# Kernel optimization log

Measured on AMD Instinct MI355X. Metric: run time of the kernel, lower is better.

## Reference

```python
import jax, jax.numpy as jnp
import numpy as np

B, S, D, H = 2, 2048, 1024, 16
HD = D // H

def setup_inputs() -> dict:
    key = jax.random.key(0)
    ks = jax.random.split(key, 9)
    s = 1.0 / np.sqrt(D)
    return {
        "x": jax.random.normal(ks[0], (B, S, D), jnp.float32),
        "Wq": jax.random.uniform(ks[1], (D, D), jnp.float32, -s, s),
        "bq": jax.random.uniform(ks[2], (D,), jnp.float32, -s, s),
        "Wk": jax.random.uniform(ks[3], (D, D), jnp.float32, -s, s),
        "bk": jax.random.uniform(ks[4], (D,), jnp.float32, -s, s),
        "Wv": jax.random.uniform(ks[5], (D, D), jnp.float32, -s, s),
        "bv": jax.random.uniform(ks[6], (D,), jnp.float32, -s, s),
        "Wo": jax.random.uniform(ks[7], (D, D), jnp.float32, -s, s),
        "bo": jax.random.uniform(ks[8], (D,), jnp.float32, -s, s),
    }

def reference(x, Wq, bq, Wk, bk, Wv, bv, Wo, bo):
    b, s, _ = x.shape
    # projections (torch Linear: y = x @ W.T + b; here W stored as [in,out])
    q = x @ Wq + bq
    k = x @ Wk + bk
    v = x @ Wv + bv
    # [b, h, s, hd]
    q = q.reshape(b, s, H, HD).transpose(0, 2, 1, 3)
    k = k.reshape(b, s, H, HD).transpose(0, 2, 1, 3)
    v = v.reshape(b, s, H, HD).transpose(0, 2, 1, 3)
    scores = jnp.einsum("bhqd,bhkd->bhqk", q, k) / jnp.sqrt(jnp.float32(HD))
    weights = jax.nn.softmax(scores, axis=-1)
    attn = jnp.einsum("bhqk,bhkd->bhqd", weights, v)
    attn = attn.transpose(0, 2, 1, 3).reshape(b, s, D)
    return attn @ Wo + bo
```

## Files before the change

kernel.cpp:

```cpp
#include <hip/hip_runtime.h>
#include <hip/hip_bf16.h>
#include <stdint.h>

#define B_  2
#define S_  2048
#define D_  1024
#define H_  16
#define HD_ 64
#define M_  (B_*S_)

typedef __attribute__((ext_vector_type(8)))  short short8;
typedef __attribute__((ext_vector_type(4)))  float f32x4;
typedef __attribute__((ext_vector_type(16))) float f32x16;

__device__ __forceinline__ unsigned short f2bf(float f) {
  union { float f; unsigned int u; } x; x.f = f;
  unsigned int r = (x.u + 0x7FFFu + ((x.u >> 16) & 1u)) >> 16;
  return (unsigned short)r;
}

__device__ __forceinline__ unsigned int pack2(float a, float b) {
  union { float f; unsigned int u; } x, y; x.f = a; y.f = b;
  return __builtin_amdgcn_perm(y.u + 0x8000u, x.u + 0x8000u, 0x07060302u);
}

typedef const __attribute__((address_space(1))) unsigned int* gas1_t;
typedef __attribute__((address_space(3))) unsigned int* las3_t;

__device__ __forceinline__ void gload_lds16(const void* g, void* l) {
  __builtin_amdgcn_global_load_lds((gas1_t)g, (las3_t)l, 16, 0, 0);
}

__global__ void k_cvt_bf16(const float* __restrict__ x, ushort* __restrict__ o, int n4) {
  int i = blockIdx.x * blockDim.x + threadIdx.x;
  int stride = gridDim.x * blockDim.x;
  for (int j = i; j < n4; j += stride) {
    float4 v = ((const float4*)x)[j];
    ushort4 u = make_ushort4(f2bf(v.x), f2bf(v.y), f2bf(v.z), f2bf(v.w));
    ((ushort4*)o)[j] = u;
  }
}

__global__ void k_transpose_w(const float* __restrict__ w0, const float* __restrict__ w1,
                              const float* __restrict__ w2, const float* __restrict__ w3,
                              ushort* __restrict__ o0, ushort* __restrict__ o1,
                              ushort* __restrict__ o2, ushort* __restrict__ o3) {
  const float* w = (blockIdx.z == 0) ? w0 : (blockIdx.z == 1) ? w1 : (blockIdx.z == 2) ? w2 : w3;
  ushort*      o = (blockIdx.z == 0) ? o0 : (blockIdx.z == 1) ? o1 : (blockIdx.z == 2) ? o2 : o3;
  __shared__ float t[32][33];
  int tx = threadIdx.x & 31, ty = threadIdx.x >> 5;
  int kt = blockIdx.y * 32, nt = blockIdx.x * 32;
  #pragma unroll
  for (int i = 0; i < 4; ++i)
    t[ty + 8 * i][tx] = w[(size_t)(kt + ty + 8 * i) * D_ + nt + tx];
  __syncthreads();
  #pragma unroll
  for (int i = 0; i < 4; ++i)
    o[(size_t)(nt + ty + 8 * i) * D_ + kt + tx] = f2bf(t[tx][ty + 8 * i]);
}

__global__ __launch_bounds__(256) void k_gemm_bt(const ushort* __restrict__ A,
                                                 const ushort* __restrict__ Bt,
                                                 const float* __restrict__ b0,
                                                 const float* __restrict__ b1,
                                                 const float* __restrict__ b2,
                                                 void* __restrict__ o0,
                                                 void* __restrict__ o1,
                                                 void* __restrict__ o2, int mode) {
  __shared__ char smem[2][32768];
  const int tid = threadIdx.x;
  const int w = tid >> 6, lane = tid & 63;
  const int g = lane >> 4, c = lane & 15;
  const int m0 = blockIdx.y * 128, n0 = blockIdx.x * 128;
  const int wm = (w >> 1) * 64, wn = (w & 1) * 64;

  f32x4 acc[4][4];
  #pragma unroll
  for (int i = 0; i < 4; ++i)
    #pragma unroll
    for (int j = 0; j < 4; ++j) acc[i][j] = 0.f;

  const char* Abase = (const char*)A + (size_t)m0 * (D_ * 2);
  const char* Bbase = (const char*)Bt + (size_t)n0 * (D_ * 2);

  auto stage = [&](int buf, int kb) {
    char* ls = &smem[buf][0];
    #pragma unroll
    for (int i = 0; i < 4; ++i) {
      int obase = w * 4096 + i * 1024;
      int ot = obase + lane * 16;
      int u = ot ^ (((ot >> 7) & 7) << 4);
      gload_lds16(Abase + (size_t)(u >> 7) * (D_ * 2) + kb * 128 + (u & 127), ls + obase);
    }
    #pragma unroll
    for (int i = 0; i < 4; ++i) {
      int obase = w * 4096 + i * 1024;
      int ot = obase + lane * 16;
      int u = ot ^ (((ot >> 7) & 7) << 4);
      gload_lds16(Bbase + (size_t)(u >> 7) * (D_ * 2) + kb * 128 + (u & 127), ls + 16384 + obase);
    }
  };

  stage(0, 0);
  int cur = 0;
  for (int kb = 0; kb < D_ / 64; ++kb) {
    __syncthreads();
    if (kb < D_ / 64 - 1) stage(cur ^ 1, kb + 1);
    const char* lsA = &smem[cur][0];
    const char* lsB = lsA + 16384;
    short8 a[4][2], b[4][2];
    #pragma unroll
    for (int f = 0; f < 4; ++f) {
      int rowA = wm + f * 16 + c;
      int rowB = wn + f * 16 + c;
      #pragma unroll
      for (int ks = 0; ks < 2; ++ks) {
        int offA = (rowA * 128 + ks * 64 + g * 16) ^ ((rowA & 7) << 4);
        int offB = (rowB * 128 + ks * 64 + g * 16) ^ ((rowB & 7) << 4);
        a[f][ks] = *(const short8*)(lsA + offA);
        b[f][ks] = *(const short8*)(lsB + offB);
      }
    }
    #pragma unroll
    for (int mf = 0; mf < 4; ++mf)
      #pragma unroll
      for (int nf = 0; nf < 4; ++nf) {
        acc[mf][nf] = __builtin_amdgcn_mfma_f32_16x16x32_bf16(a[mf][0], b[nf][0], acc[mf][nf], 0, 0, 0);
        acc[mf][nf] = __builtin_amdgcn_mfma_f32_16x16x32_bf16(a[mf][1], b[nf][1], acc[mf][nf], 0, 0, 0);
      }
    cur ^= 1;
  }

  const int sec = n0 >> 10;
  const float* bb = (mode == 1) ? b0 : (sec == 0) ? b0 : (sec == 1) ? b1 : b2;
  void* outp = (mode == 1) ? o0 : (sec == 0) ? o0 : (sec == 1) ? o1 : o2;
  #pragma unroll
  for (int nf = 0; nf < 4; ++nf) {
    int col = n0 + wn + nf * 16 + c;
    int lc = col & 1023;
    float bvv = bb[lc];
    #pragma unroll
    for (int mf = 0; mf < 4; ++mf) {
      #pragma unroll
      for (int r = 0; r < 4; ++r) {
        int tok = m0 + wm + mf * 16 + 4 * g + r;
        float v = acc[mf][nf][r] + bvv;
        if (mode == 1) {
          ((float*)outp)[(size_t)tok * D_ + col] = v;
        } else {
          if (sec == 0) v *= 0.18033688011112042f;
          int bi = tok >> 11, si = tok & 2047;
          int h = lc >> 6, hd = lc & 63;
          size_t off = (sec == 2)
            ? ((size_t)(bi * H_ + h) * HD_ + hd) * S_ + si
            : ((size_t)(bi * H_ + h) * S_ + si) * HD_ + hd;
          ((ushort*)outp)[off] = f2bf(v);
        }
      }
    }
  }
}

__global__ __launch_bounds__(512, 4) void k_attn(const ushort* __restrict__ Q,
                                                 const ushort* __restrict__ K,
                                                 const ushort* __restrict__ Vt,
                                                 ushort* __restrict__ O) {
  __shared__ __align__(16) char lds[2][2][16384];
  const int tid = threadIdx.x;
  const int w = tid >> 6, lane = tid & 63;
  const int qw = w & 3, g2 = w >> 2;
  const int tl = tid & 255;
  const int ql = lane & 31, hi = lane >> 5;
  const int bid = blockIdx.x;
  const int bh = (bid & 7) * 4 + ((bid >> 3) & 3);
  const int qc = bid >> 5;
  const int q0 = qc * 128 + qw * 32;
  const int kbase = g2 * 1024;
  const ushort* Qb = Q + (size_t)bh * S_ * HD_;
  const char* Kb2 = (const char*)(K + (size_t)bh * S_ * HD_);
  const char* Vb2 = (const char*)(Vt + (size_t)bh * HD_ * S_);

  short8 qf[4];
  #pragma unroll
  for (int t = 0; t < 4; ++t)
    qf[t] = *(const short8*)(Qb + (size_t)(q0 + ql) * HD_ + 16 * t + 8 * hi);

  short8 vones;
  #pragma unroll
  for (int i = 0; i < 8; ++i) vones[i] = (short)0x3F80;

  auto stageKV = [&](int buf, int k0n) {
    char* ls = &lds[buf][g2][0];
    #pragma unroll
    for (int i = 0; i < 2; ++i) {
      int o = tl * 16 + i * 4096;
      int u = o ^ (((o >> 7) & 7) << 4);
      gload_lds16(Kb2 + (size_t)(k0n + (u >> 7)) * 128 + (u & 127), ls + o);
    }
    #pragma unroll
    for (int i = 0; i < 2; ++i) {
      int o = tl * 16 + i * 4096;
      int u = o ^ (((o >> 7) & 7) << 4);
      gload_lds16(Vb2 + (size_t)(u >> 7) * (S_ * 2) + (size_t)k0n * 2 + (u & 127), ls + 8192 + o);
    }
  };

  f32x16 oacc[2], lacc;
  oacc[0] = 0.f; oacc[1] = 0.f; lacc = 0.f;
  float m = -1e30f;

  stageKV(0, kbase);
  int cur = 0;
  for (int kk = 0; kk < 16; ++kk) {
    __syncthreads();
    if (kk < 15) stageKV(cur ^ 1, kbase + (kk + 1) * 64);
    const char* lsK = &lds[cur][g2][0];
    const char* lsV = lsK + 8192;

    f32x16 st[2];
    #pragma unroll
    for (int n = 0; n < 2; ++n) {
      st[n] = 0.f;
      #pragma unroll
      for (int t = 0; t < 4; ++t) {
        int row = 32 * n + ql, col = 32 * t + 16 * hi;
        short8 kf = *(const short8*)(lsK + ((row * 128 + col) ^ ((row & 7) << 4)));
        st[n] = __builtin_amdgcn_mfma_f32_32x32x16_bf16(kf, qf[t], st[n], 0, 0, 0);
      }
    }

    float red[16];
    #pragma unroll
    for (int i = 0; i < 16; ++i) red[i] = fmaxf(st[0][i], st[1][i]);
    #pragma unroll
    for (int s = 8; s >= 1; s >>= 1)
      #pragma unroll
      for (int i = 0; i < s; ++i) red[i] = fmaxf(red[i], red[i + s]);
    float cmax = fmaxf(red[0], __shfl_xor(red[0], 32));

    if (!__all(cmax - m <= 8.0f)) {
      float mnew = fmaxf(m, cmax);
      float sc = exp2f(m - mnew);
      m = mnew;
      #pragma unroll
      for (int i = 0; i < 16; ++i) { oacc[0][i] *= sc; oacc[1][i] *= sc; }
      lacc[0] *= sc;
    }

    short8 pfrag[2][2];
    #pragma unroll
    for (int n = 0; n < 2; ++n) {
      unsigned int pk[4][2];
      #pragma unroll
      for (int b = 0; b < 4; ++b)
        #pragma unroll
        for (int p = 0; p < 2; ++p)
          pk[b][p] = pack2(exp2f(st[n][4 * b + 2 * p] - m), exp2f(st[n][4 * b + 2 * p + 1] - m));
      #pragma unroll
      for (int m2 = 0; m2 < 2; ++m2) {
        union { unsigned int u[4]; short8 v; } fr;
        fr.u[0] = pk[2 * m2][0];     fr.u[1] = pk[2 * m2][1];
        fr.u[2] = pk[2 * m2 + 1][0]; fr.u[3] = pk[2 * m2 + 1][1];
        pfrag[n][m2] = fr.v;
      }
    }

    #pragma unroll
    for (int n = 0; n < 2; ++n)
      #pragma unroll
      for (int m2 = 0; m2 < 2; ++m2)
        lacc = __builtin_amdgcn_mfma_f32_32x32x16_bf16(vones, pfrag[n][m2], lacc, 0, 0, 0);

    #pragma unroll
    for (int dt = 0; dt < 2; ++dt) {
      const int rb = (32 * dt + ql) * 128;
      const int sz = (ql & 7) << 4;
      #pragma unroll
      for (int n = 0; n < 2; ++n)
        #pragma unroll
        for (int m2 = 0; m2 < 2; ++m2) {
          const int cb = 64 * n + 32 * m2 + 8 * hi;
          union { struct { unsigned long long a, b; } q; short8 v; } vf;
          vf.q.a = *(const unsigned long long*)(lsV + ((rb + cb) ^ sz));
          vf.q.b = *(const unsigned long long*)(lsV + ((rb + cb + 16) ^ sz));
          oacc[dt] = __builtin_amdgcn_mfma_f32_32x32x16_bf16(vf.v, pfrag[n][m2], oacc[dt], 0, 0, 0);
        }
    }
    cur ^= 1;
  }

  float l = lacc[0];
  __syncthreads();
  float* fl = (float*)&lds[0][0][0];
  if (g2 == 1) {
    float* ob = fl + (qw * 32 + ql) * 64;
    #pragma unroll
    for (int dt = 0; dt < 2; ++dt)
      #pragma unroll
      for (int rg = 0; rg < 4; ++rg) {
        f32x4 v;
        v[0] = oacc[dt][4 * rg + 0]; v[1] = oacc[dt][4 * rg + 1];
        v[2] = oacc[dt][4 * rg + 2]; v[3] = oacc[dt][4 * rg + 3];
        *(f32x4*)(ob + dt * 32 + rg * 8 + 4 * hi) = v;
      }
    if (hi == 0) {
      fl[8192 + (qw * 32 + ql) * 2 + 0] = m;
      fl[8192 + (qw * 32 + ql) * 2 + 1] = l;
    }
  }
  __syncthreads();
  if (g2 == 0) {
    float mp = fl[8192 + (qw * 32 + ql) * 2 + 0];
    float lp = fl[8192 + (qw * 32 + ql) * 2 + 1];
    float mm = fmaxf(m, mp);
    float a  = exp2f(m - mm), ap = exp2f(mp - mm);
    float invl = 1.f / (l * a + lp * ap);
    const float* ob = fl + (qw * 32 + ql) * 64;
    const int bi = bh >> 4, h = bh & 15;
    const int tok = bi * S_ + q0 + ql;
    #pragma unroll
    for (int dt = 0; dt < 2; ++dt)
      #pragma unroll
      for (int rg = 0; rg < 4; ++rg) {
        f32x4 pv = *(const f32x4*)(ob + dt * 32 + rg * 8 + 4 * hi);
        ushort4 u;
        u.x = f2bf((oacc[dt][4 * rg + 0] * a + pv[0] * ap) * invl);
        u.y = f2bf((oacc[dt][4 * rg + 1] * a + pv[1] * ap) * invl);
        u.z = f2bf((oacc[dt][4 * rg + 2] * a + pv[2] * ap) * invl);
        u.w = f2bf((oacc[dt][4 * rg + 3] * a + pv[3] * ap) * invl);
        *(ushort4*)(O + (size_t)tok * D_ + h * 64 + dt * 32 + rg * 8 + 4 * hi) = u;
      }
  }
}

extern "C" void kernel_launch(void* const* d_in, const int* in_sizes, int n_in,
                              void* d_out, int out_size, void* d_ws, size_t ws_size,
                              hipStream_t stream) {
  const float* x  = (const float*)d_in[0];
  const float* Wq = (const float*)d_in[1];
  const float* bq = (const float*)d_in[2];
  const float* Wk = (const float*)d_in[3];
  const float* bk = (const float*)d_in[4];
  const float* Wv = (const float*)d_in[5];
  const float* bv = (const float*)d_in[6];
  const float* Wo = (const float*)d_in[7];
  const float* bo = (const float*)d_in[8];
  char* ws = (char*)d_ws;
  const size_t MB = 1024 * 1024;
  ushort* Xbf = (ushort*)(ws + 0);
  ushort* Wt3 = (ushort*)(ws + 8 * MB);
  ushort* Wto = (ushort*)(ws + 14 * MB);
  ushort* Qb  = (ushort*)(ws + 16 * MB);
  ushort* Kb  = (ushort*)(ws + 24 * MB);
  ushort* Vtb = (ushort*)(ws + 32 * MB);
  ushort* Att = (ushort*)(ws + 0);

  k_cvt_bf16<<<1024, 256, 0, stream>>>(x, Xbf, M_ * D_ / 4);
  k_transpose_w<<<dim3(32, 32, 4), 256, 0, stream>>>(
      Wq, Wk, Wv, Wo, Wt3, Wt3 + 1024 * 1024, Wt3 + 2048 * 1024, Wto);
  k_gemm_bt<<<dim3(24, 32), 256, 0, stream>>>(Xbf, Wt3, bq, bk, bv, Qb, Kb, Vtb, 0);
  k_attn<<<512, 512, 0, stream>>>(Qb, Kb, Vtb, Att);
  k_gemm_bt<<<dim3(8, 32), 256, 0, stream>>>(Att, Wto, bo, bo, bo, d_out, d_out, d_out, 1);
}
```

Before: 256.9 us.

## Process attention key tile in 32-key halves with a wider LDS swizzle

Splits the per-tile softmax and PV work into two 32-key sub-blocks that each run their own max update, exponentiation and MFMAs, which shortens live ranges and lowers register pressure. Changes the LDS XOR swizzle to mix in higher row bits to cut bank conflicts on K and V reads. Lowers the launch_bounds occupancy hint from 4 to 2, giving the compiler more registers per thread. In exchange, the online rescale check now runs twice per tile, and the lower occupancy can leave less latency hiding.

```diff
diff --git a/kernel.cpp b/kernel.cpp
--- a/kernel.cpp
+++ b/kernel.cpp
@@ -23,6 +23,8 @@
   union { float f; unsigned int u; } x, y; x.f = a; y.f = b;
   return __builtin_amdgcn_perm(y.u + 0x8000u, x.u + 0x8000u, 0x07060302u);
 }
+
+#define SW(row) ((((row) ^ ((row) >> 3)) & 7) << 4)
 
 typedef const __attribute__((address_space(1))) unsigned int* gas1_t;
 typedef __attribute__((address_space(3))) unsigned int* las3_t;
@@ -161,7 +163,7 @@
   }
 }
 
-__global__ __launch_bounds__(512, 4) void k_attn(const ushort* __restrict__ Q,
+__global__ __launch_bounds__(512, 2) void k_attn(const ushort* __restrict__ Q,
                                                  const ushort* __restrict__ K,
                                                  const ushort* __restrict__ Vt,
                                                  ushort* __restrict__ O) {
@@ -194,14 +196,16 @@
     #pragma unroll
     for (int i = 0; i < 2; ++i) {
       int o = tl * 16 + i * 4096;
-      int u = o ^ (((o >> 7) & 7) << 4);
-      gload_lds16(Kb2 + (size_t)(k0n + (u >> 7)) * 128 + (u & 127), ls + o);
+      int row = o >> 7;
+      int u = o ^ SW(row);
+      gload_lds16(Kb2 + (size_t)(k0n + row) * 128 + (u & 127), ls + o);
     }
     #pragma unroll
     for (int i = 0; i < 2; ++i) {
       int o = tl * 16 + i * 4096;
-      int u = o ^ (((o >> 7) & 7) << 4);
-      gload_lds16(Vb2 + (size_t)(u >> 7) * (S_ * 2) + (size_t)k0n * 2 + (u & 127), ls + 8192 + o);
+      int row = o >> 7;
+      int u = o ^ SW(row);
+      gload_lds16(Vb2 + (size_t)row * (S_ * 2) + (size_t)k0n * 2 + (u & 127), ls + 8192 + o);
     }
   };
 
@@ -217,74 +221,63 @@
     const char* lsK = &lds[cur][g2][0];
     const char* lsV = lsK + 8192;
 
-    f32x16 st[2];
     #pragma unroll
     for (int n = 0; n < 2; ++n) {
-      st[n] = 0.f;
+      f32x16 st = 0.f;
       #pragma unroll
       for (int t = 0; t < 4; ++t) {
-        int row = 32 * n + ql, col = 32 * t + 16 * hi;
-        short8 kf = *(const short8*)(lsK + ((row * 128 + col) ^ ((row & 7) << 4)));
-        st[n] = __builtin_amdgcn_mfma_f32_32x32x16_bf16(kf, qf[t], st[n], 0, 0, 0);
-      }
-    }
-
-    float red[16];
-    #pragma unroll
-    for (int i = 0; i < 16; ++i) red[i] = fmaxf(st[0][i], st[1][i]);
-    #pragma unroll
-    for (int s = 8; s >= 1; s >>= 1)
-      #pragma unroll
-      for (int i = 0; i < s; ++i) red[i] = fmaxf(red[i], red[i + s]);
-    float cmax = fmaxf(red[0], __shfl_xor(red[0], 32));
-
-    if (!__all(cmax - m <= 8.0f)) {
-      float mnew = fmaxf(m, cmax);
-      float sc = exp2f(m - mnew);
-      m = mnew;
-      #pragma unroll
-      for (int i = 0; i < 16; ++i) { oacc[0][i] *= sc; oacc[1][i] *= sc; }
-      lacc[0] *= sc;
-    }
-
-    short8 pfrag[2][2];
-    #pragma unroll
-    for (int n = 0; n < 2; ++n) {
-      unsigned int pk[4][2];
-      #pragma unroll
-      for (int b = 0; b < 4; ++b)
+        int row = 32 * n + ql;
+        short8 kf = *(const short8*)(lsK + row * 128 + ((32 * t + 16 * hi) ^ SW(row)));
+        st = __builtin_amdgcn_mfma_f32_32x32x16_bf16(kf, qf[t], st, 0, 0, 0);
+      }
+
+      float red[8];
+      #pragma unroll
+      for (int i = 0; i < 8; ++i) red[i] = fmaxf(st[i], st[i + 8]);
+      #pragma unroll
+      for (int s = 4; s >= 1; s >>= 1)
         #pragma unroll
-        for (int p = 0; p < 2; ++p)
-          pk[b][p] = pack2(exp2f(st[n][4 * b + 2 * p] - m), exp2f(st[n][4 * b + 2 * p + 1] - m));
+        for (int i = 0; i < s; ++i) red[i] = fmaxf(red[i], red[i + s]);
+      float cmax = fmaxf(red[0], __shfl_xor(red[0], 32));
+
+      if (!__all(cmax - m <= 8.0f)) {
+        float mnew = fmaxf(m, cmax);
+        float sc = exp2f(m - mnew);
+        m = mnew;
+        #pragma unroll
+        for (int i = 0; i < 16; ++i) { oacc[0][i] *= sc; oacc[1][i] *= sc; }
+        lacc[0] *= sc;
+      }
+
+      short8 pfrag[2];
       #pragma unroll
       for (int m2 = 0; m2 < 2; ++m2) {
         union { unsigned int u[4]; short8 v; } fr;
-        fr.u[0] = pk[2 * m2][0];     fr.u[1] = pk[2 * m2][1];
-        fr.u[2] = pk[2 * m2 + 1][0]; fr.u[3] = pk[2 * m2 + 1][1];
-        pfrag[n][m2] = fr.v;
-      }
-    }
-
-    #pragma unroll
-    for (int n = 0; n < 2; ++n)
-      #pragma unroll
-      for (int m2 = 0; m2 < 2; ++m2)
-        lacc = __builtin_amdgcn_mfma_f32_32x32x16_bf16(vones, pfrag[n][m2], lacc, 0, 0, 0);
-
-    #pragma unroll
-    for (int dt = 0; dt < 2; ++dt) {
-      const int rb = (32 * dt + ql) * 128;
-      const int sz = (ql & 7) << 4;
-      #pragma unroll
-      for (int n = 0; n < 2; ++n)
+        #pragma unroll
+        for (int b = 0; b < 2; ++b)
+          #pragma unroll
+          for (int p = 0; p < 2; ++p)
+            fr.u[2 * b + p] = pack2(exp2f(st[8 * m2 + 4 * b + 2 * p] - m),
+                                    exp2f(st[8 * m2 + 4 * b + 2 * p + 1] - m));
+        pfrag[m2] = fr.v;
+      }
+
+      lacc = __builtin_amdgcn_mfma_f32_32x32x16_bf16(vones, pfrag[0], lacc, 0, 0, 0);
+      lacc = __builtin_amdgcn_mfma_f32_32x32x16_bf16(vones, pfrag[1], lacc, 0, 0, 0);
+
+      #pragma unroll
+      for (int dt = 0; dt < 2; ++dt) {
+        const int row = 32 * dt + ql;
+        const int rb = row * 128, sz = SW(row);
         #pragma unroll
         for (int m2 = 0; m2 < 2; ++m2) {
           const int cb = 64 * n + 32 * m2 + 8 * hi;
           union { struct { unsigned long long a, b; } q; short8 v; } vf;
-          vf.q.a = *(const unsigned long long*)(lsV + ((rb + cb) ^ sz));
-          vf.q.b = *(const unsigned long long*)(lsV + ((rb + cb + 16) ^ sz));
-          oacc[dt] = __builtin_amdgcn_mfma_f32_32x32x16_bf16(vf.v, pfrag[n][m2], oacc[dt], 0, 0, 0);
+          vf.q.a = *(const unsigned long long*)(lsV + rb + ((cb) ^ sz));
+          vf.q.b = *(const unsigned long long*)(lsV + rb + ((cb + 16) ^ sz));
+          oacc[dt] = __builtin_amdgcn_mfma_f32_32x32x16_bf16(vf.v, pfrag[m2], oacc[dt], 0, 0, 0);
         }
+      }
     }
     cur ^= 1;
   }
```

New measurement: 232.9 us. -9.3%, faster.
